# Performance work log

Measured on AMD Instinct MI355X. Metric: run time of the kernel, lower is better.

Reference implementation:

```python
import jax, jax.numpy as jnp
import numpy as np

EMBED_DIM = 512
NUM_HEADS = 8
HEAD_DIM = EMBED_DIM // NUM_HEADS
SCALE = HEAD_DIM ** -0.5


def setup_inputs() -> dict:
    key = jax.random.key(0)
    ks = jax.random.split(key, 12)
    B, Nq, Nk, C = 2, 2048, 2048, EMBED_DIM
    # xavier_uniform bound for square CxC weights
    bound = float(np.sqrt(6.0 / (C + C)))
    def w(k):
        return jax.random.uniform(k, (C, C), jnp.float32, -bound, bound)
    return {
        "query": jax.random.normal(ks[0], (B, Nq, C), jnp.float32),
        "key": jax.random.normal(ks[1], (B, Nk, C), jnp.float32),
        "value": jax.random.normal(ks[2], (B, Nk, C), jnp.float32),
        "key_padding_mask": jnp.zeros((B, Nk), dtype=bool),
        "Wq": w(ks[3]), "bq": jnp.zeros((C,), jnp.float32),
        "Wk": w(ks[4]), "bk": jnp.zeros((C,), jnp.float32),
        "Wv": w(ks[5]), "bv": jnp.zeros((C,), jnp.float32),
        "Wo": w(ks[6]), "bo": jnp.zeros((C,), jnp.float32),
    }


def reference(query, key, value, key_padding_mask, Wq, bq, Wk, bk, Wv, bv, Wo, bo):
    B, Nq, C = query.shape
    Nk = key.shape[1]
    H, D = NUM_HEADS, HEAD_DIM
    # torch Linear: x @ W.T + b
    Q = (query @ Wq.T + bq).reshape(B, Nq, H, D).transpose(0, 2, 1, 3)  # (B,H,Nq,D)
    K = (key @ Wk.T + bk).reshape(B, Nk, H, D).transpose(0, 2, 1, 3)
    V = (value @ Wv.T + bv).reshape(B, Nk, H, D).transpose(0, 2, 1, 3)
    scores = jnp.einsum("bhqd,bhkd->bhqk", Q, K) * SCALE  # (B,H,Nq,Nk)
    scores = jnp.where(key_padding_mask[:, None, None, :], -jnp.inf, scores)
    attn = jax.nn.softmax(scores, axis=-1)
    out = jnp.einsum("bhqk,bhkd->bhqd", attn, V)  # (B,H,Nq,D)
    out = out.transpose(0, 2, 1, 3).reshape(B, Nq, C)
    return out @ Wo.T + bo
```

## Files before the change

### kernel.cpp

```cpp
#include <hip/hip_runtime.h>

typedef unsigned short u16;
typedef __attribute__((ext_vector_type(8))) short short8;
typedef __attribute__((ext_vector_type(8))) __bf16 bf16x8;
typedef __attribute__((ext_vector_type(4))) float f32x4;
typedef __attribute__((ext_vector_type(4))) unsigned int u32x4;

#define MFMA_BF16(a, b, c) __builtin_amdgcn_mfma_f32_16x16x32_bf16((a), (b), (c), 0, 0, 0)

__device__ __forceinline__ u16 f2bf(float f) {
    unsigned u = __builtin_bit_cast(unsigned, f);
    u += 0x7FFFu + ((u >> 16) & 1u);
    return (u16)(u >> 16);
}

__device__ __forceinline__ unsigned pack_bf2(float lo, float hi) {
    return (unsigned)f2bf(lo) | ((unsigned)f2bf(hi) << 16);
}

__global__ __launch_bounds__(256) void proj_gemm(
    const float* __restrict__ Xq, const float* __restrict__ Xk, const float* __restrict__ Xv,
    const float* __restrict__ Wq, const float* __restrict__ Wk, const float* __restrict__ Wv,
    const float* __restrict__ bq, const float* __restrict__ bk, const float* __restrict__ bv,
    u16* __restrict__ Oq, u16* __restrict__ Ok, u16* __restrict__ Ov)
{
    constexpr int K = 512, N = 512;
    const int z = blockIdx.z;
    const float* __restrict__ X = (z == 0) ? Xq : (z == 1) ? Xk : Xv;
    const float* __restrict__ W = (z == 0) ? Wq : (z == 1) ? Wk : Wv;
    const float* __restrict__ bias = (z == 0) ? bq : (z == 1) ? bk : bv;
    u16* __restrict__ O = (z == 0) ? Oq : (z == 1) ? Ok : Ov;
    const float alpha = (z == 0) ? 0.125f * 1.44269504088896f : 1.0f;

    __shared__ u16 lA[128 * 64];
    __shared__ u16 lB[128 * 64];

    const int tid = threadIdx.x, lane = tid & 63, w = tid >> 6;
    const int wr = w >> 1, wc = w & 1;
    const int bm = blockIdx.x, bn = blockIdx.y;
    const int r0 = tid >> 3, cc = tid & 7;

    f32x4 acc[4][4];
    for (int m = 0; m < 4; ++m)
        for (int n = 0; n < 4; ++n)
            acc[m][n] = f32x4{0.f, 0.f, 0.f, 0.f};

    for (int kt = 0; kt < K; kt += 64) {
        __syncthreads();
        for (int p = 0; p < 4; ++p) {
            int r = r0 + p * 32;
            {
                const float4* g = (const float4*)(X + (size_t)(bm * 128 + r) * K + kt + cc * 8);
                float4 f0 = g[0], f1 = g[1];
                short8 v;
                v[0] = (short)f2bf(f0.x); v[1] = (short)f2bf(f0.y);
                v[2] = (short)f2bf(f0.z); v[3] = (short)f2bf(f0.w);
                v[4] = (short)f2bf(f1.x); v[5] = (short)f2bf(f1.y);
                v[6] = (short)f2bf(f1.z); v[7] = (short)f2bf(f1.w);
                *(short8*)&lA[r * 64 + ((cc ^ (r & 7)) << 3)] = v;
            }
            {
                const float4* g = (const float4*)(W + (size_t)(bn * 128 + r) * K + kt + cc * 8);
                float4 f0 = g[0], f1 = g[1];
                short8 v;
                v[0] = (short)f2bf(f0.x); v[1] = (short)f2bf(f0.y);
                v[2] = (short)f2bf(f0.z); v[3] = (short)f2bf(f0.w);
                v[4] = (short)f2bf(f1.x); v[5] = (short)f2bf(f1.y);
                v[6] = (short)f2bf(f1.z); v[7] = (short)f2bf(f1.w);
                *(short8*)&lB[r * 64 + ((cc ^ (r & 7)) << 3)] = v;
            }
        }
        __syncthreads();
        for (int kk = 0; kk < 2; ++kk) {
            bf16x8 af[4], bfr[4];
            for (int m = 0; m < 4; ++m) {
                int row = wr * 64 + m * 16 + (lane & 15);
                af[m] = *(const bf16x8*)&lA[row * 64 + (((kk * 4 + (lane >> 4)) ^ (row & 7)) << 3)];
            }
            for (int n = 0; n < 4; ++n) {
                int row = wc * 64 + n * 16 + (lane & 15);
                bfr[n] = *(const bf16x8*)&lB[row * 64 + (((kk * 4 + (lane >> 4)) ^ (row & 7)) << 3)];
            }
            for (int m = 0; m < 4; ++m)
                for (int n = 0; n < 4; ++n)
                    acc[m][n] = MFMA_BF16(af[m], bfr[n], acc[m][n]);
        }
    }
    for (int m = 0; m < 4; ++m)
        for (int n = 0; n < 4; ++n) {
            int row = bm * 128 + wr * 64 + m * 16 + ((lane >> 4) << 2);
            int col = bn * 128 + wc * 64 + n * 16 + (lane & 15);
            float bv_ = bias[col];
            for (int i = 0; i < 4; ++i) {
                float v = (acc[m][n][i] + bv_) * alpha;
                O[(size_t)(row + i) * N + col] = f2bf(v);
            }
        }
}

__global__ __launch_bounds__(256) void out_gemm(
    const u16* __restrict__ A, const float* __restrict__ W,
    const float* __restrict__ bias, float* __restrict__ O)
{
    constexpr int K = 512, N = 512;
    __shared__ u16 lA[128 * 64];
    __shared__ u16 lB[128 * 64];

    const int tid = threadIdx.x, lane = tid & 63, w = tid >> 6;
    const int wr = w >> 1, wc = w & 1;
    const int bm = blockIdx.x, bn = blockIdx.y;
    const int r0 = tid >> 3, cc = tid & 7;

    f32x4 acc[4][4];
    for (int m = 0; m < 4; ++m)
        for (int n = 0; n < 4; ++n)
            acc[m][n] = f32x4{0.f, 0.f, 0.f, 0.f};

    for (int kt = 0; kt < K; kt += 64) {
        __syncthreads();
        for (int p = 0; p < 4; ++p) {
            int r = r0 + p * 32;
            *(short8*)&lA[r * 64 + ((cc ^ (r & 7)) << 3)] =
                *(const short8*)(A + (size_t)(bm * 128 + r) * K + kt + cc * 8);
            const float4* g = (const float4*)(W + (size_t)(bn * 128 + r) * K + kt + cc * 8);
            float4 f0 = g[0], f1 = g[1];
            short8 v;
            v[0] = (short)f2bf(f0.x); v[1] = (short)f2bf(f0.y);
            v[2] = (short)f2bf(f0.z); v[3] = (short)f2bf(f0.w);
            v[4] = (short)f2bf(f1.x); v[5] = (short)f2bf(f1.y);
            v[6] = (short)f2bf(f1.z); v[7] = (short)f2bf(f1.w);
            *(short8*)&lB[r * 64 + ((cc ^ (r & 7)) << 3)] = v;
        }
        __syncthreads();
        for (int kk = 0; kk < 2; ++kk) {
            bf16x8 af[4], bfr[4];
            for (int m = 0; m < 4; ++m) {
                int row = wr * 64 + m * 16 + (lane & 15);
                af[m] = *(const bf16x8*)&lA[row * 64 + (((kk * 4 + (lane >> 4)) ^ (row & 7)) << 3)];
            }
            for (int n = 0; n < 4; ++n) {
                int row = wc * 64 + n * 16 + (lane & 15);
                bfr[n] = *(const bf16x8*)&lB[row * 64 + (((kk * 4 + (lane >> 4)) ^ (row & 7)) << 3)];
            }
            for (int m = 0; m < 4; ++m)
                for (int n = 0; n < 4; ++n)
                    acc[m][n] = MFMA_BF16(af[m], bfr[n], acc[m][n]);
        }
    }
    for (int m = 0; m < 4; ++m)
        for (int n = 0; n < 4; ++n) {
            int row = bm * 128 + wr * 64 + m * 16 + ((lane >> 4) << 2);
            int col = bn * 128 + wc * 64 + n * 16 + (lane & 15);
            float bv_ = bias[col];
            for (int i = 0; i < 4; ++i)
                O[(size_t)(row + i) * N + col] = acc[m][n][i] + bv_;
        }
}

__global__ __launch_bounds__(256) void attn_k(
    const u16* __restrict__ Qp, const u16* __restrict__ Kp, const u16* __restrict__ Vp,
    const unsigned char* __restrict__ mask, u16* __restrict__ Ob)
{
    constexpr int C = 512, NK = 2048, NT = NK / 64;
    __shared__ u16 lK[2][64 * 64];
    __shared__ u16 lV[2][64 * 64];

    const int tid = threadIdx.x, lane = tid & 63, w = tid >> 6;
    const int gd = lane >> 4, q15 = lane & 15;
    const int bh = blockIdx.x, qb = blockIdx.y;
    const int b = bh >> 3, h = bh & 7;
    const size_t qrow0 = (size_t)b * 2048 + qb * 64;
    const size_t krow0 = (size_t)b * 2048;
    const int col0 = h * 64;
    const int rs = tid >> 3, cc = tid & 7;

    bf16x8 qf[2];
    {
        const u16* qrow = Qp + (qrow0 + w * 16 + q15) * C + col0;
        qf[0] = *(const bf16x8*)(qrow + gd * 8);
        qf[1] = *(const bf16x8*)(qrow + 32 + gd * 8);
    }

    float mst = -1e30f, lst = 0.f;
    f32x4 oacc[4];
    #pragma unroll
    for (int i = 0; i < 4; ++i) oacc[i] = f32x4{0.f, 0.f, 0.f, 0.f};

    #pragma unroll
    for (int p = 0; p < 2; ++p) {
        int r = rs + p * 32;
        *(short8*)&lK[0][r * 64 + ((cc ^ (r & 7)) << 3)] =
            *(const short8*)(Kp + (krow0 + r) * C + col0 + cc * 8);
        short8 vv = *(const short8*)(Vp + (krow0 + r) * C + col0 + cc * 8);
        #pragma unroll
        for (int j = 0; j < 8; ++j)
            lV[0][(cc * 8 + j) * 64 + ((((r >> 3) ^ ((j + cc) & 7))) << 3) + (r & 7)] = (u16)vv[j];
    }
    __syncthreads();

    int cur = 0;
    for (int t = 0; t < NT; ++t) {
        const int kv = t * 64;
        const bool hasnext = (t + 1 < NT);
        short8 kreg[2], vreg[2];
        if (hasnext) {
            #pragma unroll
            for (int p = 0; p < 2; ++p) {
                int r = rs + p * 32;
                kreg[p] = *(const short8*)(Kp + (krow0 + kv + 64 + r) * C + col0 + cc * 8);
                vreg[p] = *(const short8*)(Vp + (krow0 + kv + 64 + r) * C + col0 + cc * 8);
            }
        }
        unsigned char mbyte = mask[(size_t)b * NK + kv + lane];

        f32x4 s[4];
        #pragma unroll
        for (int i = 0; i < 4; ++i) s[i] = f32x4{0.f, 0.f, 0.f, 0.f};
        const u16* Kc = &lK[cur][0];
        __builtin_amdgcn_s_setprio(1);
        #pragma unroll
        for (int kb = 0; kb < 2; ++kb)
            #pragma unroll
            for (int t4 = 0; t4 < 4; ++t4) {
                int krow = t4 * 16 + q15;
                bf16x8 kf = *(const bf16x8*)&Kc[krow * 64 + (((kb * 4 + gd) ^ (krow & 7)) << 3)];
                s[t4] = MFMA_BF16(kf, qf[kb], s[t4]);
            }
        __builtin_amdgcn_s_setprio(0);

        unsigned long long mb = __ballot(mbyte != 0);
        if (mb) {
            #pragma unroll
            for (int t4 = 0; t4 < 4; ++t4)
                #pragma unroll
                for (int i = 0; i < 4; ++i) {
                    int k = t4 * 16 + gd * 4 + i;
                    if ((mb >> k) & 1ull) s[t4][i] = -1e30f;
                }
        }

        float pmax = s[0][0];
        #pragma unroll
        for (int t4 = 0; t4 < 4; ++t4)
            #pragma unroll
            for (int i = 0; i < 4; ++i) pmax = fmaxf(pmax, s[t4][i]);
        pmax = fmaxf(pmax, __shfl_xor(pmax, 16));
        pmax = fmaxf(pmax, __shfl_xor(pmax, 32));

        if (!__all(pmax - mst <= 11.0f)) {
            float mn = fmaxf(mst, pmax);
            float sf = exp2f(mst - mn);
            mst = mn;
            lst *= sf;
            #pragma unroll
            for (int i = 0; i < 4; ++i) {
                float sfi = __shfl(sf, (lane & 48) | ((gd << 2) + i));
                #pragma unroll
                for (int t2 = 0; t2 < 4; ++t2) oacc[t2][i] *= sfi;
            }
        }

        float p[4][4];
        float rsum = 0.f;
        #pragma unroll
        for (int t4 = 0; t4 < 4; ++t4)
            #pragma unroll
            for (int i = 0; i < 4; ++i) {
                float e = exp2f(s[t4][i] - mst);
                p[t4][i] = e;
                rsum += e;
            }
        rsum += __shfl_xor(rsum, 16);
        rsum += __shfl_xor(rsum, 32);
        lst += rsum;

        const u16* Vc = &lV[cur][0];
        __builtin_amdgcn_s_setprio(1);
        #pragma unroll
        for (int kb = 0; kb < 2; ++kb) {
            u32x4 pw;
            pw[0] = pack_bf2(p[2 * kb][0], p[2 * kb][1]);
            pw[1] = pack_bf2(p[2 * kb][2], p[2 * kb][3]);
            pw[2] = pack_bf2(p[2 * kb + 1][0], p[2 * kb + 1][1]);
            pw[3] = pack_bf2(p[2 * kb + 1][2], p[2 * kb + 1][3]);
            bf16x8 pa = __builtin_bit_cast(bf16x8, pw);
            #pragma unroll
            for (int t2 = 0; t2 < 4; ++t2) {
                int d = t2 * 16 + q15;
                int swd = (d + (d >> 3)) & 7;
                int base = d * 64 + 4 * (gd & 1);
                uint2 v0 = *(const uint2*)&Vc[base + (((4 * kb + 0 + (gd >> 1)) ^ swd) << 3)];
                uint2 v1 = *(const uint2*)&Vc[base + (((4 * kb + 2 + (gd >> 1)) ^ swd) << 3)];
                u32x4 vw; vw[0] = v0.x; vw[1] = v0.y; vw[2] = v1.x; vw[3] = v1.y;
                bf16x8 vf = __builtin_bit_cast(bf16x8, vw);
                oacc[t2] = MFMA_BF16(pa, vf, oacc[t2]);
            }
        }
        __builtin_amdgcn_s_setprio(0);

        if (hasnext) {
            int nxt = cur ^ 1;
            #pragma unroll
            for (int p = 0; p < 2; ++p) {
                int r = rs + p * 32;
                *(short8*)&lK[nxt][r * 64 + ((cc ^ (r & 7)) << 3)] = kreg[p];
                #pragma unroll
                for (int j = 0; j < 8; ++j)
                    lV[nxt][(cc * 8 + j) * 64 + ((((r >> 3) ^ ((j + cc) & 7))) << 3) + (r & 7)] = (u16)vreg[p][j];
            }
            __syncthreads();
            cur = nxt;
        }
    }

    #pragma unroll
    for (int i = 0; i < 4; ++i) {
        float li = __shfl(lst, (lane & 48) | ((gd << 2) + i));
        float inv = 1.f / li;
        int qg = qb * 64 + w * 16 + gd * 4 + i;
        #pragma unroll
        for (int t2 = 0; t2 < 4; ++t2) {
            int col = col0 + t2 * 16 + q15;
            Ob[((size_t)b * 2048 + qg) * C + col] = f2bf(oacc[t2][i] * inv);
        }
    }
}

extern "C" void kernel_launch(void* const* d_in, const int* in_sizes, int n_in,
                              void* d_out, int out_size, void* d_ws, size_t ws_size,
                              hipStream_t stream) {
    const float* query = (const float*)d_in[0];
    const float* key   = (const float*)d_in[1];
    const float* value = (const float*)d_in[2];
    const unsigned char* mask = (const unsigned char*)d_in[3];
    const float* Wq = (const float*)d_in[4];
    const float* bq = (const float*)d_in[5];
    const float* Wk = (const float*)d_in[6];
    const float* bk = (const float*)d_in[7];
    const float* Wv = (const float*)d_in[8];
    const float* bv = (const float*)d_in[9];
    const float* Wo = (const float*)d_in[10];
    const float* bo = (const float*)d_in[11];

    u16* ws = (u16*)d_ws;
    u16* Qp = ws;
    u16* Kp = ws + 2097152;
    u16* Vp = ws + 4194304;
    u16* Ob = ws + 6291456;

    dim3 gp(32, 4, 3);
    proj_gemm<<<gp, 256, 0, stream>>>(query, key, value, Wq, Wk, Wv, bq, bk, bv, Qp, Kp, Vp);

    dim3 ga(16, 32);
    attn_k<<<ga, 256, 0, stream>>>(Qp, Kp, Vp, mask, Ob);

    dim3 go(32, 4);
    out_gemm<<<go, 256, 0, stream>>>(Ob, Wo, bo, (float*)d_out);
}
```

Baseline: 87.55 us.

## Process 128-key tiles per sync, defer row-sum reduction, use native exp/cvt

The attention kernel now loads and double-buffers two 64-key K/V subtiles per iteration, which halves the number of barriers and global prefetch rounds but doubles LDS use. The per-row sum reduction is deferred to a single cross-lane reduction at the end. The row-max shuffle runs only when a rescale is needed. Software bf16 rounding and exp2f are replaced by the v_cvt_pk_bf16_f32 and v_exp_f32 instructions. The larger LDS footprint (64KB) and extra prefetch registers may lower occupancy.

```diff
diff --git a/kernel.cpp b/kernel.cpp
--- a/kernel.cpp
+++ b/kernel.cpp
@@ -14,8 +14,16 @@
     return (u16)(u >> 16);
 }
 
-__device__ __forceinline__ unsigned pack_bf2(float lo, float hi) {
-    return (unsigned)f2bf(lo) | ((unsigned)f2bf(hi) << 16);
+__device__ __forceinline__ unsigned cvt_pk_bf16(float lo, float hi) {
+    unsigned r;
+    asm("v_cvt_pk_bf16_f32 %0, %1, %2" : "=v"(r) : "v"(lo), "v"(hi));
+    return r;
+}
+
+__device__ __forceinline__ float fast_exp2(float x) {
+    float r;
+    asm("v_exp_f32 %0, %1" : "=v"(r) : "v"(x));
+    return r;
 }
 
 __global__ __launch_bounds__(256) void proj_gemm(
@@ -161,9 +169,9 @@
     const u16* __restrict__ Qp, const u16* __restrict__ Kp, const u16* __restrict__ Vp,
     const unsigned char* __restrict__ mask, u16* __restrict__ Ob)
 {
-    constexpr int C = 512, NK = 2048, NT = NK / 64;
-    __shared__ u16 lK[2][64 * 64];
-    __shared__ u16 lV[2][64 * 64];
+    constexpr int C = 512, NK = 2048, NP = NK / 128;
+    __shared__ u16 lK[2][2][64 * 64];
+    __shared__ u16 lV[2][2][64 * 64];
 
     const int tid = threadIdx.x, lane = tid & 63, w = tid >> 6;
     const int gd = lane >> 4, q15 = lane & 15;
@@ -181,141 +189,167 @@
         qf[1] = *(const bf16x8*)(qrow + 32 + gd * 8);
     }
 
-    float mst = -1e30f, lst = 0.f;
+    float mst = -1e30f, lstp = 0.f;
     f32x4 oacc[4];
     #pragma unroll
     for (int i = 0; i < 4; ++i) oacc[i] = f32x4{0.f, 0.f, 0.f, 0.f};
 
-    #pragma unroll
-    for (int p = 0; p < 2; ++p) {
-        int r = rs + p * 32;
-        *(short8*)&lK[0][r * 64 + ((cc ^ (r & 7)) << 3)] =
-            *(const short8*)(Kp + (krow0 + r) * C + col0 + cc * 8);
-        short8 vv = *(const short8*)(Vp + (krow0 + r) * C + col0 + cc * 8);
-        #pragma unroll
-        for (int j = 0; j < 8; ++j)
-            lV[0][(cc * 8 + j) * 64 + ((((r >> 3) ^ ((j + cc) & 7))) << 3) + (r & 7)] = (u16)vv[j];
-    }
-    __syncthreads();
-
-    int cur = 0;
-    for (int t = 0; t < NT; ++t) {
-        const int kv = t * 64;
-        const bool hasnext = (t + 1 < NT);
-        short8 kreg[2], vreg[2];
-        if (hasnext) {
+    {
+        short8 kr[2][2], vr[2][2];
+        #pragma unroll
+        for (int u = 0; u < 2; ++u)
             #pragma unroll
             for (int p = 0; p < 2; ++p) {
                 int r = rs + p * 32;
-                kreg[p] = *(const short8*)(Kp + (krow0 + kv + 64 + r) * C + col0 + cc * 8);
-                vreg[p] = *(const short8*)(Vp + (krow0 + kv + 64 + r) * C + col0 + cc * 8);
-            }
-        }
-        unsigned char mbyte = mask[(size_t)b * NK + kv + lane];
-
-        f32x4 s[4];
-        #pragma unroll
-        for (int i = 0; i < 4; ++i) s[i] = f32x4{0.f, 0.f, 0.f, 0.f};
-        const u16* Kc = &lK[cur][0];
+                kr[u][p] = *(const short8*)(Kp + (krow0 + u * 64 + r) * C + col0 + cc * 8);
+                vr[u][p] = *(const short8*)(Vp + (krow0 + u * 64 + r) * C + col0 + cc * 8);
+            }
+        #pragma unroll
+        for (int u = 0; u < 2; ++u)
+            #pragma unroll
+            for (int p = 0; p < 2; ++p) {
+                int r = rs + p * 32;
+                *(short8*)&lK[0][u][r * 64 + ((cc ^ (r & 7)) << 3)] = kr[u][p];
+                #pragma unroll
+                for (int j = 0; j < 8; ++j)
+                    lV[0][u][(cc * 8 + j) * 64 + (((r >> 3) ^ ((j + cc) & 7)) << 3) + (r & 7)] = (u16)vr[u][p][j];
+            }
+    }
+    __syncthreads();
+
+    int cur = 0;
+    for (int pj = 0; pj < NP; ++pj) {
+        const int kv = pj * 128;
+        const bool hasnext = (pj + 1 < NP);
+        short8 kreg[2][2], vreg[2][2];
+        if (hasnext) {
+            #pragma unroll
+            for (int u = 0; u < 2; ++u)
+                #pragma unroll
+                for (int p = 0; p < 2; ++p) {
+                    int r = rs + p * 32;
+                    kreg[u][p] = *(const short8*)(Kp + (krow0 + kv + 128 + u * 64 + r) * C + col0 + cc * 8);
+                    vreg[u][p] = *(const short8*)(Vp + (krow0 + kv + 128 + u * 64 + r) * C + col0 + cc * 8);
+                }
+        }
+        unsigned char mby[2];
+        mby[0] = mask[(size_t)b * NK + kv + lane];
+        mby[1] = mask[(size_t)b * NK + kv + 64 + lane];
+
+        f32x4 s2[2][4];
+        #pragma unroll
+        for (int u = 0; u < 2; ++u)
+            #pragma unroll
+            for (int i = 0; i < 4; ++i) s2[u][i] = f32x4{0.f, 0.f, 0.f, 0.f};
         __builtin_amdgcn_s_setprio(1);
         #pragma unroll
-        for (int kb = 0; kb < 2; ++kb)
-            #pragma unroll
-            for (int t4 = 0; t4 < 4; ++t4) {
-                int krow = t4 * 16 + q15;
-                bf16x8 kf = *(const bf16x8*)&Kc[krow * 64 + (((kb * 4 + gd) ^ (krow & 7)) << 3)];
-                s[t4] = MFMA_BF16(kf, qf[kb], s[t4]);
-            }
+        for (int u = 0; u < 2; ++u) {
+            const u16* Kc = &lK[cur][u][0];
+            #pragma unroll
+            for (int kb = 0; kb < 2; ++kb)
+                #pragma unroll
+                for (int t4 = 0; t4 < 4; ++t4) {
+                    int krow = t4 * 16 + q15;
+                    bf16x8 kf = *(const bf16x8*)&Kc[krow * 64 + (((kb * 4 + gd) ^ (krow & 7)) << 3)];
+                    s2[u][t4] = MFMA_BF16(kf, qf[kb], s2[u][t4]);
+                }
+        }
         __builtin_amdgcn_s_setprio(0);
 
-        unsigned long long mb = __ballot(mbyte != 0);
-        if (mb) {
+        #pragma unroll
+        for (int u = 0; u < 2; ++u) {
+            unsigned long long m64 = __ballot(mby[u] != 0);
+            if (m64) {
+                #pragma unroll
+                for (int t4 = 0; t4 < 4; ++t4)
+                    #pragma unroll
+                    for (int i = 0; i < 4; ++i) {
+                        int k = t4 * 16 + gd * 4 + i;
+                        if ((m64 >> k) & 1ull) s2[u][t4][i] = -1e30f;
+                    }
+            }
+
+            float pmax = s2[u][0][0];
             #pragma unroll
             for (int t4 = 0; t4 < 4; ++t4)
                 #pragma unroll
+                for (int i = 0; i < 4; ++i) pmax = fmaxf(pmax, s2[u][t4][i]);
+
+            if (!__all(pmax - mst <= 11.0f)) {
+                float rm = fmaxf(pmax, __shfl_xor(pmax, 16));
+                rm = fmaxf(rm, __shfl_xor(rm, 32));
+                float mn = fmaxf(mst, rm);
+                float sf = exp2f(mst - mn);
+                mst = mn;
+                lstp *= sf;
+                #pragma unroll
                 for (int i = 0; i < 4; ++i) {
-                    int k = t4 * 16 + gd * 4 + i;
-                    if ((mb >> k) & 1ull) s[t4][i] = -1e30f;
-                }
-        }
-
-        float pmax = s[0][0];
-        #pragma unroll
-        for (int t4 = 0; t4 < 4; ++t4)
-            #pragma unroll
-            for (int i = 0; i < 4; ++i) pmax = fmaxf(pmax, s[t4][i]);
-        pmax = fmaxf(pmax, __shfl_xor(pmax, 16));
-        pmax = fmaxf(pmax, __shfl_xor(pmax, 32));
-
-        if (!__all(pmax - mst <= 11.0f)) {
-            float mn = fmaxf(mst, pmax);
-            float sf = exp2f(mst - mn);
-            mst = mn;
-            lst *= sf;
-            #pragma unroll
-            for (int i = 0; i < 4; ++i) {
-                float sfi = __shfl(sf, (lane & 48) | ((gd << 2) + i));
-                #pragma unroll
-                for (int t2 = 0; t2 < 4; ++t2) oacc[t2][i] *= sfi;
-            }
-        }
-
-        float p[4][4];
-        float rsum = 0.f;
-        #pragma unroll
-        for (int t4 = 0; t4 < 4; ++t4)
-            #pragma unroll
-            for (int i = 0; i < 4; ++i) {
-                float e = exp2f(s[t4][i] - mst);
-                p[t4][i] = e;
-                rsum += e;
-            }
-        rsum += __shfl_xor(rsum, 16);
-        rsum += __shfl_xor(rsum, 32);
-        lst += rsum;
-
-        const u16* Vc = &lV[cur][0];
-        __builtin_amdgcn_s_setprio(1);
-        #pragma unroll
-        for (int kb = 0; kb < 2; ++kb) {
-            u32x4 pw;
-            pw[0] = pack_bf2(p[2 * kb][0], p[2 * kb][1]);
-            pw[1] = pack_bf2(p[2 * kb][2], p[2 * kb][3]);
-            pw[2] = pack_bf2(p[2 * kb + 1][0], p[2 * kb + 1][1]);
-            pw[3] = pack_bf2(p[2 * kb + 1][2], p[2 * kb + 1][3]);
-            bf16x8 pa = __builtin_bit_cast(bf16x8, pw);
-            #pragma unroll
-            for (int t2 = 0; t2 < 4; ++t2) {
-                int d = t2 * 16 + q15;
-                int swd = (d + (d >> 3)) & 7;
-                int base = d * 64 + 4 * (gd & 1);
-                uint2 v0 = *(const uint2*)&Vc[base + (((4 * kb + 0 + (gd >> 1)) ^ swd) << 3)];
-                uint2 v1 = *(const uint2*)&Vc[base + (((4 * kb + 2 + (gd >> 1)) ^ swd) << 3)];
-                u32x4 vw; vw[0] = v0.x; vw[1] = v0.y; vw[2] = v1.x; vw[3] = v1.y;
-                bf16x8 vf = __builtin_bit_cast(bf16x8, vw);
-                oacc[t2] = MFMA_BF16(pa, vf, oacc[t2]);
-            }
-        }
-        __builtin_amdgcn_s_setprio(0);
+                    float sfi = __shfl(sf, (lane & 48) | ((gd << 2) + i));
+                    #pragma unroll
+                    for (int t2 = 0; t2 < 4; ++t2) oacc[t2][i] *= sfi;
+                }
+            }
+
+            float p[4][4];
+            float rsum = 0.f;
+            #pragma unroll
+            for (int t4 = 0; t4 < 4; ++t4)
+                #pragma unroll
+                for (int i = 0; i < 4; ++i) {
+                    float e = fast_exp2(s2[u][t4][i] - mst);
+                    p[t4][i] = e;
+                    rsum += e;
+                }
+            lstp += rsum;
+
+            const u16* Vc = &lV[cur][u][0];
+            __builtin_amdgcn_s_setprio(1);
+            #pragma unroll
+            for (int kb = 0; kb < 2; ++kb) {
+                u32x4 pw;
+                pw[0] = cvt_pk_bf16(p[2 * kb][0], p[2 * kb][1]);
+                pw[1] = cvt_pk_bf16(p[2 * kb][2], p[2 * kb][3]);
+                pw[2] = cvt_pk_bf16(p[2 * kb + 1][0], p[2 * kb + 1][1]);
+                pw[3] = cvt_pk_bf16(p[2 * kb + 1][2], p[2 * kb + 1][3]);
+                bf16x8 pa = __builtin_bit_cast(bf16x8, pw);
+                #pragma unroll
+                for (int t2 = 0; t2 < 4; ++t2) {
+                    int d = t2 * 16 + q15;
+                    int swd = (d + (d >> 3)) & 7;
+                    int base = d * 64 + 4 * (gd & 1);
+                    uint2 v0 = *(const uint2*)&Vc[base + (((4 * kb + 0 + (gd >> 1)) ^ swd) << 3)];
+                    uint2 v1 = *(const uint2*)&Vc[base + (((4 * kb + 2 + (gd >> 1)) ^ swd) << 3)];
+                    u32x4 vw; vw[0] = v0.x; vw[1] = v0.y; vw[2] = v1.x; vw[3] = v1.y;
+                    bf16x8 vf = __builtin_bit_cast(bf16x8, vw);
+                    oacc[t2] = MFMA_BF16(pa, vf, oacc[t2]);
+                }
+            }
+            __builtin_amdgcn_s_setprio(0);
+        }
 
         if (hasnext) {
             int nxt = cur ^ 1;
             #pragma unroll
-            for (int p = 0; p < 2; ++p) {
-                int r = rs + p * 32;
-                *(short8*)&lK[nxt][r * 64 + ((cc ^ (r & 7)) << 3)] = kreg[p];
-                #pragma unroll
-                for (int j = 0; j < 8; ++j)
-                    lV[nxt][(cc * 8 + j) * 64 + ((((r >> 3) ^ ((j + cc) & 7))) << 3) + (r & 7)] = (u16)vreg[p][j];
-            }
+            for (int u = 0; u < 2; ++u)
+                #pragma unroll
+                for (int p = 0; p < 2; ++p) {
+                    int r = rs + p * 32;
+                    *(short8*)&lK[nxt][u][r * 64 + ((cc ^ (r & 7)) << 3)] = kreg[u][p];
+                    #pragma unroll
+                    for (int j = 0; j < 8; ++j)
+                        lV[nxt][u][(cc * 8 + j) * 64 + (((r >> 3) ^ ((j + cc) & 7)) << 3) + (r & 7)] = (u16)vreg[u][p][j];
+                }
             __syncthreads();
             cur = nxt;
         }
     }
 
+    float lsum = lstp + __shfl_xor(lstp, 16);
+    lsum += __shfl_xor(lsum, 32);
+
     #pragma unroll
     for (int i = 0; i < 4; ++i) {
-        float li = __shfl(lst, (lane & 48) | ((gd << 2) + i));
+        float li = __shfl(lsum, (lane & 48) | ((gd << 2) + i));
         float inv = 1.f / li;
         int qg = qb * 64 + w * 16 + gd * 4 + i;
         #pragma unroll
```

After: 72.37 us. -17.3%, faster.
